# Optimization experiments

Hardware: AMD Instinct MI355X
Metric: run time of the kernel (lower is better)

## Reference

```python
import jax, jax.numpy as jnp
import numpy as np

V_THRESHOLD = 0.5
V_RESET = 0.0
TAU = 5.0
ALPHA = 0.1
BETA = 0.5
SURROGATE_PARAM = 2.0

# Heaviside spike with sigmoid surrogate gradient (ActFun.apply equivalent)
@jax.custom_vjp
def spike_fn(x):
    return (x > 0).astype(x.dtype)

def _spike_fwd(x):
    return spike_fn(x), x

def _spike_bwd(x, g):
    s = jax.nn.sigmoid(SURROGATE_PARAM * x)
    return (g * SURROGATE_PARAM * s * (1.0 - s),)

spike_fn.defvjp(_spike_fwd, _spike_bwd)


def setup_inputs() -> dict:
    key = jax.random.key(0)
    B, T, N = 32, 64, 32768
    X = jax.random.normal(key, (B, T, N), dtype=jnp.float32)
    return {"X": X}


def reference(X):
    # X: [B, T, N]; sequential LIF recurrence over T with cache term
    init = jnp.zeros_like(X[:, 0])  # mem and cache start at 0

    def step(carry, x_t):
        mem, cache = carry
        mem = mem / TAU + (1.0 + ALPHA * cache) * x_t
        spike = spike_fn(mem - V_THRESHOLD)
        mem = (1.0 - spike) * mem + V_RESET * spike  # hard reset (v_reset=0.0)
        cache = BETA * cache + (1.0 - spike)
        return (mem, cache), spike

    X_t = jnp.moveaxis(X, 1, 0)  # [T, B, N]
    _, spikes = jax.lax.scan(step, (init, init), X_t)
    return jnp.moveaxis(spikes, 0, 1)  # [B, T, N]
```

## Files before the change

### kernel.cpp

```cpp
#include <hip/hip_runtime.h>


constexpr int B = 32;
constexpr int T = 64;
constexpr int N = 32768;
constexpr int NTHREADS = B * N;

__global__ __launch_bounds__(256) void lif_kernel(const float* __restrict__ X,
                                                  float* __restrict__ out) {
#pragma clang fp contract(off)
    const int i = blockIdx.x * blockDim.x + threadIdx.x;
    const int b = i >> 15;
    const int n = i & (N - 1);
    const int base = b * (T * N) + n;

    const float* __restrict__ Xp = X + base;
    float* __restrict__ Op = out + base;

    float xs[T];
#pragma unroll
    for (int t = 0; t < T; ++t) {
        xs[t] = Xp[t * N];
    }

    __builtin_amdgcn_sched_barrier(0);

    float mem = 0.f, ca = 0.f;
#pragma unroll
    for (int t = 0; t < T; ++t) {
        float m = mem / 5.0f + (1.0f + 0.1f * ca) * xs[t];
        float s = ((m - 0.5f) > 0.0f) ? 1.0f : 0.0f;
        mem = (1.0f - s) * m;
        ca = 0.5f * ca + (1.0f - s);
        Op[t * N] = s;
    }
}

extern "C" void kernel_launch(void* const* d_in, const int* in_sizes, int n_in,
                              void* d_out, int out_size, void* d_ws, size_t ws_size,
                              hipStream_t stream) {
    const float* X = (const float*)d_in[0];
    float* out = (float*)d_out;
    const int block = 256;
    const int grid = NTHREADS / block;
    lif_kernel<<<grid, block, 0, stream>>>(X, out);
}
```

Baseline: 427.5 us.

## Double-buffer time-step loads in 16-step chunks and raise occupancy hint

Replaces the load-all-64-then-compute structure with two 16-element register buffers. While the current chunk is computed, the buffers are refilled with later time steps, so loads overlap with compute and stores. This cuts register pressure from 64 input values to 32, and the launch bounds now request 8 waves per EU for higher occupancy. The risk is that fewer loads are in flight per thread, and the sched barriers may limit how the compiler interleaves work.

```diff
diff --git a/kernel.cpp b/kernel.cpp
--- a/kernel.cpp
+++ b/kernel.cpp
@@ -6,8 +6,8 @@
 constexpr int N = 32768;
 constexpr int NTHREADS = B * N;
 
-__global__ __launch_bounds__(256) void lif_kernel(const float* __restrict__ X,
-                                                  float* __restrict__ out) {
+__global__ __launch_bounds__(256, 8) void lif_kernel(const float* __restrict__ X,
+                                                     float* __restrict__ out) {
 #pragma clang fp contract(off)
     const int i = blockIdx.x * blockDim.x + threadIdx.x;
     const int b = i >> 15;
@@ -17,23 +17,52 @@
     const float* __restrict__ Xp = X + base;
     float* __restrict__ Op = out + base;
 
-    float xs[T];
+    float mem = 0.f, ca = 0.f;
+
+    float xs0[16], xs1[16];
+
 #pragma unroll
-    for (int t = 0; t < T; ++t) {
-        xs[t] = Xp[t * N];
+    for (int j = 0; j < 16; ++j) xs0[j] = Xp[j * N];
+#pragma unroll
+    for (int j = 0; j < 16; ++j) xs1[j] = Xp[(16 + j) * N];
+    __builtin_amdgcn_sched_barrier(0);
+
+#define LIFSTEP(xv, t)                                        \
+    {                                                         \
+        float m_ = mem / 5.0f + (1.0f + 0.1f * ca) * (xv);    \
+        float s_ = ((m_ - 0.5f) > 0.0f) ? 1.0f : 0.0f;        \
+        mem = (1.0f - s_) * m_;                               \
+        ca = 0.5f * ca + (1.0f - s_);                         \
+        Op[(t) * N] = s_;                                     \
     }
 
+#pragma unroll
+    for (int j = 0; j < 16; ++j) {
+        const float xv = xs0[j];
+        xs0[j] = Xp[(32 + j) * N];
+        LIFSTEP(xv, j)
+    }
     __builtin_amdgcn_sched_barrier(0);
 
-    float mem = 0.f, ca = 0.f;
 #pragma unroll
-    for (int t = 0; t < T; ++t) {
-        float m = mem / 5.0f + (1.0f + 0.1f * ca) * xs[t];
-        float s = ((m - 0.5f) > 0.0f) ? 1.0f : 0.0f;
-        mem = (1.0f - s) * m;
-        ca = 0.5f * ca + (1.0f - s);
-        Op[t * N] = s;
+    for (int j = 0; j < 16; ++j) {
+        const float xv = xs1[j];
+        xs1[j] = Xp[(48 + j) * N];
+        LIFSTEP(xv, 16 + j)
     }
+    __builtin_amdgcn_sched_barrier(0);
+
+#pragma unroll
+    for (int j = 0; j < 16; ++j) {
+        LIFSTEP(xs0[j], 32 + j)
+    }
+    __builtin_amdgcn_sched_barrier(0);
+
+#pragma unroll
+    for (int j = 0; j < 16; ++j) {
+        LIFSTEP(xs1[j], 48 + j)
+    }
+#undef LIFSTEP
 }
 
 extern "C" void kernel_launch(void* const* d_in, const int* in_sizes, int n_in,
```

Result: no change. 430.4 us (+0.7%).
